# Performance work log

Hardware: AMD Instinct MI355X
Metric: run time of the kernel (lower is better)

The kernel has to match this reference:

```python
import jax, jax.numpy as jnp
import numpy as np

B, H_IMG, W_IMG, C_IMG, NP = 8, 384, 384, 3, 6
DELTA = 10
TOL = 1e-3
LAM = 0.05          # lambda_ (Charbonnier scale)
MAX_ITER = 12
RIDGE = 1e-6


def _cubic(s):
    # Keys bicubic convolution kernel, a = -0.5
    a = -0.5
    s = jnp.abs(s)
    s2 = s * s
    s3 = s2 * s
    w1 = (a + 2.0) * s3 - (a + 3.0) * s2 + 1.0
    w2 = a * s3 - 5.0 * a * s2 + 8.0 * a * s - 4.0 * a
    return jnp.where(s <= 1.0, w1, jnp.where(s < 2.0, w2, 0.0))


def _bicubic(I, xg, yg):
    # I: [b,H,W,C]; xg,yg: [b,H,W] sample coordinates
    Bn, Hh, Ww, C = I.shape
    x0 = jnp.floor(xg)
    y0 = jnp.floor(yg)
    tx = xg - x0
    ty = yg - y0
    xi = x0.astype(jnp.int32)
    yi = y0.astype(jnp.int32)
    bidx = jnp.arange(Bn)[:, None, None]
    out = jnp.zeros(I.shape, I.dtype)
    for j in range(4):           # fixed 4x4 tap stencil
        wy = _cubic(ty - (j - 1))
        yy = jnp.clip(yi + (j - 1), 0, Hh - 1)
        for k in range(4):
            wx = _cubic(tx - (k - 1))
            xx = jnp.clip(xi + (k - 1), 0, Ww - 1)
            out = out + (wy * wx)[..., None] * I[bidx, yy, xx, :]
    return out


def _params2matrix(p):
    # AFFINITY: x' = x + p0 + p2*x + p3*y ; y' = y + p1 + p4*x + p5*y
    zero = jnp.zeros_like(p[:, 0])
    one = jnp.ones_like(p[:, 0])
    r0 = jnp.stack([1.0 + p[:, 2], p[:, 3], p[:, 0]], -1)
    r1 = jnp.stack([p[:, 4], 1.0 + p[:, 5], p[:, 1]], -1)
    r2 = jnp.stack([zero, zero, one], -1)
    return jnp.stack([r0, r1, r2], 1)


def _matrix2params(M):
    M = M / M[:, 2:3, 2:3]
    return jnp.stack([M[:, 0, 2], M[:, 1, 2], M[:, 0, 0] - 1.0,
                      M[:, 0, 1], M[:, 1, 0], M[:, 1, 1] - 1.0], -1)


def _gradients(I):
    # central differences, zero-padded at the borders (as in compute_gradients)
    Ix = jnp.pad((I[:, :, 2:, :] - I[:, :, :-2, :]) * 0.5,
                 ((0, 0), (0, 0), (1, 1), (0, 0)))
    Iy = jnp.pad((I[:, 2:, :, :] - I[:, :-2, :, :]) * 0.5,
                 ((0, 0), (1, 1), (0, 0), (0, 0)))
    return Ix, Iy


def setup_inputs() -> dict:
    key = jax.random.key(0)
    k1, k2 = jax.random.split(key)
    I1 = jax.random.uniform(k1, (B, H_IMG, W_IMG, C_IMG), jnp.float32)
    I2 = jax.random.uniform(k2, (B, H_IMG, W_IMG, C_IMG), jnp.float32)
    p = jnp.zeros((B, NP), jnp.float32)
    return {"I1": I1, "I2": I2, "p": p}


def _forward(I1, I2, p):
    Bn, Hh, Ww, C = I1.shape
    x = jnp.arange(Ww, dtype=jnp.float32)
    y = jnp.arange(Hh, dtype=jnp.float32)
    X, Y = jnp.meshgrid(x, y)
    ones = jnp.ones_like(X)
    zeros = jnp.zeros_like(X)
    # AFFINITY Jacobian, split into Jx / Jy halves: [H,W,6]
    Jx = jnp.stack([ones, zeros, X, Y, zeros, zeros], -1)
    Jy = jnp.stack([zeros, ones, zeros, zeros, X, Y], -1)
    Ix, Iy = _gradients(I1)
    # steepest-descent images: [b,H,W,C,6]
    DIJ = Ix[..., None] * Jx[None, :, :, None, :] + Iy[..., None] * Jy[None, :, :, None, :]
    rows_ok = (jnp.arange(Hh) >= DELTA) & (jnp.arange(Hh) < Hh - DELTA)
    cols_ok = (jnp.arange(Ww) >= DELTA) & (jnp.arange(Ww) < Ww - DELTA)
    valid1 = (rows_ok[:, None] & cols_ok[None, :])[None, :, :, None]  # [1,H,W,1]
    coords = jnp.stack([X, Y, ones], 0)  # [3,H,W]
    eye = jnp.eye(NP, dtype=jnp.float32)

    def warp(pcur):
        M = _params2matrix(pcur)
        g = jnp.einsum('bij,jhw->bihw', M, coords)
        xg, yg = g[:, 0], g[:, 1]
        Iw = _bicubic(I2, xg, yg)
        gx = jnp.round(xg).astype(jnp.int32)
        gy = jnp.round(yg).astype(jnp.int32)
        wmask = ((gx >= DELTA) & (gx <= Ww - DELTA) &
                 (gy >= DELTA) & (gy <= Hh - DELTA))[..., None]
        return Iw, wmask

    def step(carry, _):
        pcur, done = carry
        Iw, wmask = carry_warp = warp(pcur)
        m = wmask & valid1
        DI = jnp.where(m, Iw - I1, 0.0)
        # Charbonnier influence weight psi(e) = 1/sqrt(1 + (e/lam)^2)
        w = jnp.where(m, jax.lax.rsqrt(1.0 + (DI / LAM) ** 2), 0.0)
        bvec = jnp.einsum('bhwcm,bhwc->bm', DIJ, w * DI)
        Hm = jnp.einsum('bhwcm,bhwcn->bmn', DIJ * w[..., None], DIJ)
        dp = jnp.linalg.solve(Hm + RIDGE * eye, bvec[..., None])[..., 0]
        # inverse-compositional update: W(p) <- W(p) o W(dp)^-1
        Mn = _params2matrix(pcur) @ jnp.linalg.inv(_params2matrix(dp))
        p_new = _matrix2params(Mn)
        conv = jnp.linalg.norm(dp, axis=-1) < TOL
        p_out = jnp.where(done[:, None], pcur, p_new)
        return (p_out, done | conv), None

    (pf, _), _ = jax.lax.scan(step, (p, jnp.zeros((Bn,), bool)), None, length=MAX_ITER)
    Iw, wmask = warp(pf)
    m = wmask & valid1
    DI = jnp.where(m, Iw - I1, 0.0)
    rho = 2.0 * LAM * LAM * (jnp.sqrt(1.0 + (DI / LAM) ** 2) - 1.0)
    mb = jnp.broadcast_to(m, DI.shape)
    cnt = jnp.sum(mb.astype(jnp.float32), axis=(1, 2, 3))
    err = jnp.sum(jnp.where(mb, rho, 0.0), axis=(1, 2, 3)) / jnp.maximum(cnt, 1.0)
    return pf, err, DI, Iw


def reference(I1, I2, p):
    return _forward(I1, I2, p)
```

## Files before the change

### kernel.cpp

```cpp
#include <hip/hip_runtime.h>
#include <math.h>

#define BB 8
#define HH 384
#define WW 384
#define NPAR 6
#define DEL 10
#define MAXIT 12
#define NACC 24
#define HWPIX (HH*WW)
#define NRT4 91
#define NWIN 6
#define NBX (NRT4*NWIN)
#define L1N 91
#define L1CNT (6*BB)
#define CNTS 92
#define NR2F 6
#define PITCHF 141
#define WSF 140
#define KB_ 8
#define SPS 32

typedef float vf4 __attribute__((ext_vector_type(4)));
typedef vf4 uvf4 __attribute__((aligned(4)));
typedef float f2v __attribute__((ext_vector_type(2), aligned(4)));
typedef float lf4 __attribute__((ext_vector_type(4)));

__device__ __forceinline__ vf4 ldv4(const float* p) { return *(const uvf4*)p; }

__device__ __forceinline__ lf4 ldpx3(const float* __restrict__ Ib, int pixoff) {
    const int fo = pixoff * 3;
    if (fo + 4 <= HWPIX * 3) {
        vf4 v = ldv4(Ib + fo);
        return (lf4){v.x, v.y, v.z, 0.f};
    }
    vf4 v = ldv4(Ib + fo - 1);
    return (lf4){v.y, v.z, v.w, 0.f};
}

__device__ __forceinline__ float cubicw(float s) {
    s = fabsf(s);
    float s2 = s * s, s3 = s2 * s;
    float w1 = 1.5f * s3 - 2.5f * s2 + 1.0f;
    float w2 = -0.5f * s3 + 2.5f * s2 - 4.0f * s + 2.0f;
    return (s <= 1.0f) ? w1 : ((s < 2.0f) ? w2 : 0.0f);
}

__device__ __forceinline__ void bicubic3_fast(const float* __restrict__ Ib, double xg, double yg, float Iw[3]) {
    double fx = floor(xg), fy = floor(yg);
    float tx = (float)(xg - fx), ty = (float)(yg - fy);
    int xi = (int)fx, yi = (int)fy;
    float wx[4], wyv[4];
#pragma unroll
    for (int k = 0; k < 4; k++) { wx[k] = cubicw(tx - (float)(k - 1)); wyv[k] = cubicw(ty - (float)(k - 1)); }
    Iw[0] = 0.f; Iw[1] = 0.f; Iw[2] = 0.f;
    const float* base = Ib + (yi - 1) * (WW * 3) + (xi - 1) * 3;
#pragma unroll
    for (int j = 0; j < 4; j++) {
        const float* r = base + j * (WW * 3);
        vf4 v0 = ldv4(r), v1 = ldv4(r + 4), v2 = ldv4(r + 8);
        float r0 = fmaf(wx[0], v0.x, 0.f); r0 = fmaf(wx[1], v0.w, r0); r0 = fmaf(wx[2], v1.z, r0); r0 = fmaf(wx[3], v2.y, r0);
        float r1 = fmaf(wx[0], v0.y, 0.f); r1 = fmaf(wx[1], v1.x, r1); r1 = fmaf(wx[2], v1.w, r1); r1 = fmaf(wx[3], v2.z, r1);
        float r2 = fmaf(wx[0], v0.z, 0.f); r2 = fmaf(wx[1], v1.y, r2); r2 = fmaf(wx[2], v2.x, r2); r2 = fmaf(wx[3], v2.w, r2);
        Iw[0] = fmaf(wyv[j], r0, Iw[0]);
        Iw[1] = fmaf(wyv[j], r1, Iw[1]);
        Iw[2] = fmaf(wyv[j], r2, Iw[2]);
    }
}

__device__ __forceinline__ void bicubic3_gen(const float* __restrict__ Ib, double xg, double yg, float Iw[3]) {
    double fx = floor(xg), fy = floor(yg);
    int xi = (int)fx, yi = (int)fy;
    float tx = (float)(xg - fx), ty = (float)(yg - fy);
    float wx[4], wyv[4];
    int xx[4], yy[4];
#pragma unroll
    for (int k = 0; k < 4; k++) {
        wx[k] = cubicw(tx - (float)(k - 1)); wyv[k] = cubicw(ty - (float)(k - 1));
        xx[k] = min(max(xi + k - 1, 0), WW - 1);
        yy[k] = min(max(yi + k - 1, 0), HH - 1);
    }
    Iw[0] = 0.f; Iw[1] = 0.f; Iw[2] = 0.f;
#pragma unroll
    for (int j = 0; j < 4; j++) {
        const float* row = Ib + yy[j] * (WW * 3);
        float r0 = 0.f, r1 = 0.f, r2 = 0.f;
#pragma unroll
        for (int k = 0; k < 4; k++) {
            const float* q = row + xx[k] * 3;
            r0 = fmaf(wx[k], q[0], r0); r1 = fmaf(wx[k], q[1], r1); r2 = fmaf(wx[k], q[2], r2);
        }
        Iw[0] = fmaf(wyv[j], r0, Iw[0]);
        Iw[1] = fmaf(wyv[j], r1, Iw[1]);
        Iw[2] = fmaf(wyv[j], r2, Iw[2]);
    }
}

template<int P>
__device__ __forceinline__ void bicubic3_lds(const lf4* __restrict__ T, int ssx, int ssy,
                                             float tx, float ty, float Iw[3]) {
    float wx[4], wyv[4];
#pragma unroll
    for (int k = 0; k < 4; k++) { wx[k] = cubicw(tx - (float)(k - 1)); wyv[k] = cubicw(ty - (float)(k - 1)); }
    Iw[0] = 0.f; Iw[1] = 0.f; Iw[2] = 0.f;
    const lf4* bp = T + (ssy - 1) * P + (ssx - 1);
#pragma unroll
    for (int j = 0; j < 4; j++) {
        lf4 t0 = bp[j * P + 0], t1 = bp[j * P + 1], t2 = bp[j * P + 2], t3 = bp[j * P + 3];
        float r0 = fmaf(wx[0], t0.x, 0.f); r0 = fmaf(wx[1], t1.x, r0); r0 = fmaf(wx[2], t2.x, r0); r0 = fmaf(wx[3], t3.x, r0);
        float r1 = fmaf(wx[0], t0.y, 0.f); r1 = fmaf(wx[1], t1.y, r1); r1 = fmaf(wx[2], t2.y, r1); r1 = fmaf(wx[3], t3.y, r1);
        float r2 = fmaf(wx[0], t0.z, 0.f); r2 = fmaf(wx[1], t1.z, r2); r2 = fmaf(wx[2], t2.z, r2); r2 = fmaf(wx[3], t3.z, r2);
        Iw[0] = fmaf(wyv[j], r0, Iw[0]);
        Iw[1] = fmaf(wyv[j], r1, Iw[1]);
        Iw[2] = fmaf(wyv[j], r2, Iw[2]);
    }
}

__device__ __forceinline__
void solve6_fast(const double* __restrict__ Sb, const double* __restrict__ pc,
                 double pn[6], int* convp) {
    const double b0 = Sb[0], b1 = Sb[3], b2 = Sb[1], b3 = Sb[2], b4 = Sb[4], b5 = Sb[5];
    const double h00 = Sb[6]  + 1e-6, h01 = Sb[12], h02 = Sb[7],  h03 = Sb[8],  h04 = Sb[13], h05 = Sb[14];
    const double h11 = Sb[18] + 1e-6, h12 = Sb[13], h13 = Sb[14], h14 = Sb[19], h15 = Sb[20];
    const double h22 = Sb[9]  + 1e-6, h23 = Sb[10], h24 = Sb[15], h25 = Sb[16];
    const double h33 = Sb[11] + 1e-6, h34 = Sb[16], h35 = Sb[17];
    const double h44 = Sb[21] + 1e-6, h45 = Sb[22];
    const double h55 = Sb[23] + 1e-6;

    const double l00 = sqrt(h00);
    const double i0 = 1.0 / l00;
    const double l10 = h01 * i0, l20 = h02 * i0, l30 = h03 * i0, l40 = h04 * i0, l50 = h05 * i0;
    const double l11 = sqrt(h11 - l10 * l10);
    const double i1 = 1.0 / l11;
    const double l21 = (h12 - l20 * l10) * i1;
    const double l31 = (h13 - l30 * l10) * i1;
    const double l41 = (h14 - l40 * l10) * i1;
    const double l51 = (h15 - l50 * l10) * i1;
    const double l22 = sqrt(h22 - l20 * l20 - l21 * l21);
    const double i2 = 1.0 / l22;
    const double l32 = (h23 - l30 * l20 - l31 * l21) * i2;
    const double l42 = (h24 - l40 * l20 - l41 * l21) * i2;
    const double l52 = (h25 - l50 * l20 - l51 * l21) * i2;
    const double l33 = sqrt(h33 - l30 * l30 - l31 * l31 - l32 * l32);
    const double i3 = 1.0 / l33;
    const double l43 = (h34 - l40 * l30 - l41 * l31 - l42 * l32) * i3;
    const double l53 = (h35 - l50 * l30 - l51 * l31 - l52 * l32) * i3;
    const double l44 = sqrt(h44 - l40 * l40 - l41 * l41 - l42 * l42 - l43 * l43);
    const double i4 = 1.0 / l44;
    const double l54 = (h45 - l50 * l40 - l51 * l41 - l52 * l42 - l53 * l43) * i4;
    const double l55 = sqrt(h55 - l50 * l50 - l51 * l51 - l52 * l52 - l53 * l53 - l54 * l54);
    const double i5 = 1.0 / l55;

    const double y0 = b0 * i0;
    const double y1 = (b1 - l10 * y0) * i1;
    const double y2 = (b2 - l20 * y0 - l21 * y1) * i2;
    const double y3 = (b3 - l30 * y0 - l31 * y1 - l32 * y2) * i3;
    const double y4 = (b4 - l40 * y0 - l41 * y1 - l42 * y2 - l43 * y3) * i4;
    const double y5 = (b5 - l50 * y0 - l51 * y1 - l52 * y2 - l53 * y3 - l54 * y4) * i5;

    const double d5 = y5 * i5;
    const double d4 = (y4 - l54 * d5) * i4;
    const double d3 = (y3 - l43 * d4 - l53 * d5) * i3;
    const double d2 = (y2 - l32 * d3 - l42 * d4 - l52 * d5) * i2;
    const double d1 = (y1 - l21 * d2 - l31 * d3 - l41 * d4 - l51 * d5) * i1;
    const double d0 = (y0 - l10 * d1 - l20 * d2 - l30 * d3 - l40 * d4 - l50 * d5) * i0;

    const double nrm = sqrt(d0*d0 + d1*d1 + d2*d2 + d3*d3 + d4*d4 + d5*d5);
    *convp = (nrm < 1e-3) ? 1 : 0;

    const double m00 = 1.0 + pc[2], m01 = pc[3], m02 = pc[0];
    const double m10 = pc[4], m11 = 1.0 + pc[5], m12 = pc[1];
    const double q00 = 1.0 + d2, q01 = d3, q02 = d0;
    const double q10 = d4, q11 = 1.0 + d5, q12 = d1;
    const double det = q00 * q11 - q01 * q10;
    const double j00 = q11 / det, j01 = -q01 / det;
    const double j10 = -q10 / det, j11 = q00 / det;
    const double jt0 = -(j00 * q02 + j01 * q12);
    const double jt1 = -(j10 * q02 + j11 * q12);
    const double n00 = m00 * j00 + m01 * j10;
    const double n01 = m00 * j01 + m01 * j11;
    const double n02 = m00 * jt0 + m01 * jt1 + m02;
    const double n10 = m10 * j00 + m11 * j10;
    const double n11 = m10 * j01 + m11 * j11;
    const double n12 = m10 * jt0 + m11 * jt1 + m12;
    pn[0] = n02;
    pn[1] = n12;
    pn[2] = n00 - 1.0;
    pn[3] = n01;
    pn[4] = n10;
    pn[5] = n11 - 1.0;
}

extern "C" __global__ __launch_bounds__(256)
void k_init(const float* __restrict__ p0, double* __restrict__ p_store,
            int* __restrict__ done0, double* __restrict__ S_part_all,
            double* __restrict__ Sf_part, unsigned int* __restrict__ cnt) {
    const int idx = blockIdx.x * 256 + threadIdx.x;
    const int n = MAXIT * KB_ * BB * SPS;
    for (int i = idx; i < n; i += gridDim.x * 256) S_part_all[i] = 0.0;
    for (int i = idx; i < MAXIT * CNTS; i += gridDim.x * 256) cnt[i] = 0u;
    if (blockIdx.x == 0) {
        const int tid = threadIdx.x;
        if (tid < KB_ * BB * 4) Sf_part[tid] = 0.0;
        if (tid < BB * NPAR) p_store[tid] = (double)p0[tid];
        if (tid < BB) done0[tid] = 0;
    }
}

extern "C" __global__ __launch_bounds__(256, 8)
void k_iter(const float* __restrict__ I1, const float* __restrict__ I2,
            const double* __restrict__ p_in, const int* __restrict__ done_in,
            double* __restrict__ S_out, double* __restrict__ p_out,
            int* __restrict__ done_out, unsigned int* __restrict__ c1,
            unsigned int* __restrict__ c2) {
    __shared__ __align__(16) double SMEMD[1664];
    __shared__ int lastflag;
    double* scr = SMEMD;
    const int tid = threadIdx.x;
    const int b = blockIdx.y;
    const int tix = blockIdx.x;
    const int dn = done_in[b];

    if (!dn) {
        const int rt = tix / NWIN, win = tix - rt * NWIN;
        const int y0 = 10 + rt * 4;
        const int x0 = 10 + win * 64;

        double pp[NPAR];
#pragma unroll
        for (int i = 0; i < NPAR; i++) pp[i] = p_in[b * NPAR + i];
        const double M00 = 1.0 + pp[2], M01 = pp[3], M02 = pp[0];
        const double M10 = pp[4], M11 = 1.0 + pp[5], M12 = pp[1];
        const float* I1b = I1 + (size_t)b * HWPIX * 3;
        const float* I2b = I2 + (size_t)b * HWPIX * 3;

        const int wid = tid >> 6, lane = tid & 63;
        const int y = y0 + wid;
        const double Y = (double)y;
        const double Bx = M01 * Y + M02;
        const double By = M11 * Y + M12;
        const int x = x0 + lane;
        const double X = (double)x;
        const double xg = fma(M00, X, Bx);
        const double yg = fma(M10, X, By);
        const double gx = rint(xg), gy = rint(yg);
        const bool ok = (x < WW - DEL) &&
                        (gx >= (double)DEL && gx <= (double)(WW - DEL) &&
                         gy >= (double)DEL && gy <= (double)(HH - DEL));

        float Iw[3];
        if (ok) {
            bicubic3_fast(I2b, xg, yg, Iw);
        } else {
            Iw[0] = 0.f; Iw[1] = 0.f; Iw[2] = 0.f;
        }

        const int xc = min(x, WW - DEL - 1);
        const int pixL = y * WW + xc;
        const float* c = I1b + pixL * 3;
        vf4 u0 = ldv4(c - 3);
        vf4 u1 = ldv4(c + 1);
        float cr2 = c[5];
        vf4 uu = ldv4(c - WW * 3);
        vf4 ud = ldv4(c + WW * 3);

        const float cl[3] = {u0.x, u0.y, u0.z};
        const float cv[3] = {u0.w, u1.x, u1.y};
        const float cr[3] = {u1.z, u1.w, cr2};
        const float cu[3] = {uu.x, uu.y, uu.z};
        const float cd[3] = {ud.x, ud.y, ud.z};

        const float msk = ok ? 1.0f : 0.0f;
        float Af = 0.f, Bf = 0.f, Cf = 0.f, T0f = 0.f, T1f = 0.f;
#pragma unroll
        for (int ch = 0; ch < 3; ch++) {
            const float Ix = (cr[ch] - cl[ch]) * 0.5f;
            const float Iy = (cd[ch] - cu[ch]) * 0.5f;
            const float d = Iw[ch] - cv[ch];
            const float u = d * 20.0f;
            const float w = msk / sqrtf(fmaf(u, u, 1.0f));
            const float wd = w * d;
            T0f = fmaf(Ix, wd, T0f);
            T1f = fmaf(Iy, wd, T1f);
            const float wIx = w * Ix;
            Af = fmaf(wIx, Ix, Af);
            Bf = fmaf(wIx, Iy, Bf);
            Cf = fmaf(w * Iy, Iy, Cf);
        }
        const double T0 = (double)T0f, T1 = (double)T1f;
        const double A = (double)Af, Bd = (double)Bf, Cd = (double)Cf;
        const double XX = X * X;
        double s[13];
        s[0] = T0;  s[1] = T0 * X;
        s[2] = T1;  s[3] = T1 * X;
        s[4] = A;   s[5] = A * X;   s[6] = A * XX;
        s[7] = Bd;  s[8] = Bd * X;  s[9] = Bd * XX;
        s[10] = Cd; s[11] = Cd * X; s[12] = Cd * XX;

#pragma unroll
        for (int i = 0; i < 13; i++) s[i] += __shfl_down(s[i], 32, 64);

        if (lane < 32) {
            double* o = scr + ((size_t)(wid * 32 + lane)) * 13;
#pragma unroll
            for (int i = 0; i < 13; i++) o[i] = s[i];
        }
        __syncthreads();

        if (tid < NACC) {
            const unsigned long long CLO = 0x9787456454232010ULL;
            const unsigned long long CHI = 0x00000000abcaba78ULL;
            const unsigned long long YPW = 0x0000910910910410ULL;
            const int cix = (int)(((tid < 16) ? (CLO >> (tid * 4)) : (CHI >> ((tid - 16) * 4))) & 0xF);
            const int pw  = (int)((YPW >> (tid * 2)) & 0x3);
            double acc = 0.0;
            for (int w = 0; w < 4; w++) {
                const double* basep = scr + ((size_t)(w * 32)) * 13 + cix;
                double part = 0.0;
                for (int l = 0; l < 32; l++) part += basep[(size_t)l * 13];
                const double Yw = (double)(y0 + w);
                const double f = (pw == 0) ? 1.0 : ((pw == 1) ? Yw : Yw * Yw);
                acc = fma(f, part, acc);
            }
            const int bkt = tix & (KB_ - 1);
            double oldv = unsafeAtomicAdd(&S_out[((size_t)(bkt * BB + b)) * SPS + tid], acc);
            asm volatile("" :: "v"(oldv));
        }
    }

    __syncthreads();
    if (tid == 0) {
        lastflag = 0;
        const unsigned o1 = __hip_atomic_fetch_add(&c1[tix % L1N], 1u,
                                __ATOMIC_RELAXED, __HIP_MEMORY_SCOPE_AGENT);
        if (o1 == (unsigned)(L1CNT - 1)) {
            const unsigned o2 = __hip_atomic_fetch_add(c2, 1u,
                                    __ATOMIC_RELAXED, __HIP_MEMORY_SCOPE_AGENT);
            if (o2 == (unsigned)(L1N - 1)) lastflag = 1;
        }
    }
    __syncthreads();
    if (lastflag) {
        double* FSUM = SMEMD;
        if (tid < BB * NACC) {
            const int bt = tid / NACC, a = tid - bt * NACC;
            double sv = 0.0;
#pragma unroll
            for (int k = 0; k < KB_; k++)
                sv += __hip_atomic_load(&S_out[((size_t)(k * BB + bt)) * SPS + a],
                                        __ATOMIC_RELAXED, __HIP_MEMORY_SCOPE_AGENT);
            FSUM[bt * NACC + a] = sv;
        }
        __syncthreads();
        if (tid < BB) {
            const int bt = tid;
            double pc[NPAR], pn[NPAR];
#pragma unroll
            for (int i = 0; i < NPAR; i++) pc[i] = p_in[bt * NPAR + i];
            if (done_in[bt]) {
#pragma unroll
                for (int i = 0; i < NPAR; i++) p_out[bt * NPAR + i] = pc[i];
                done_out[bt] = 1;
            } else {
                int conv;
                solve6_fast(&FSUM[bt * NACC], pc, pn, &conv);
#pragma unroll
                for (int i = 0; i < NPAR; i++) p_out[bt * NPAR + i] = pn[i];
                done_out[bt] = conv;
            }
        }
    }
}

extern "C" __global__ __launch_bounds__(256, 8)
void k_final_map(const float* __restrict__ I1, const float* __restrict__ I2,
                 const double* __restrict__ pf_in,
                 float* __restrict__ DI_out, float* __restrict__ Iw_out,
                 double* __restrict__ Sf_part) {
    __shared__ lf4 I2S[NR2F * PITCHF];
    __shared__ double wsum[4][2];
    const int tid = threadIdx.x;
    const int b = blockIdx.y;
    const int tix = blockIdx.x;
    const int rt = tix / 3, win = tix - rt * 3;
    const int y0 = rt * 2;
    const int x0 = win * 128;
    const int sx0 = x0 - 6;

    double pp[NPAR];
#pragma unroll
    for (int i = 0; i < NPAR; i++) pp[i] = pf_in[b * NPAR + i];
    const double M00 = 1.0 + pp[2], M01 = pp[3], M02 = pp[0];
    const double M10 = pp[4], M11 = 1.0 + pp[5], M12 = pp[1];
    const float* I1b = I1 + (size_t)b * HWPIX * 3;
    const float* I2b = I2 + (size_t)b * HWPIX * 3;
    float* DIb = DI_out + (size_t)b * HWPIX * 3;
    float* Iwb = Iw_out + (size_t)b * HWPIX * 3;

    const double ygc = M10 * (double)(x0 + 64) + M11 * ((double)y0 + 0.5) + M12;
    const int r0 = (int)fmin(fmax(floor(ygc) - 2.0, -100000.0), 100000.0);
    for (int i = tid; i < NR2F * WSF; i += 256) {
        const int r = i / WSF, c = i - r * WSF;
        const int gr = min(max(r0 + r, 0), HH - 1);
        const int gc = min(max(sx0 + c, 0), WW - 1);
        I2S[r * PITCHF + c] = ldpx3(I2b, gr * WW + gc);
    }
    __syncthreads();

    const int row = tid >> 7;
    const int x = x0 + (tid & 127);
    const int y = y0 + row;
    const int pix = y * WW + x;

    const double X = (double)x, Yd = (double)y;
    const double xg = fma(M00, X, fma(M01, Yd, M02));
    const double yg = fma(M10, X, fma(M11, Yd, M12));
    const double fx = floor(xg), fy = floor(yg);
    const int xi = (int)fx, yi = (int)fy;
    const float tx = (float)(xg - fx), ty = (float)(yg - fy);
    const int sxi = xi - sx0, syi = yi - r0;
    const bool inwin = (sxi >= 1) && (sxi <= WSF - 3) && (syi >= 1) && (syi <= NR2F - 3);

    float Iwp[3];
    if (inwin) bicubic3_lds<PITCHF>(I2S, sxi, syi, tx, ty, Iwp);
    else       bicubic3_gen(I2b, xg, yg, Iwp);

    const bool v1 = (x >= DEL) && (x < WW - DEL) && (y >= DEL) && (y < HH - DEL);
    const double gx = rint(xg), gy = rint(yg);
    const bool wm = (gx >= (double)DEL && gx <= (double)(WW - DEL) &&
                     gy >= (double)DEL && gy <= (double)(HH - DEL));
    const bool mp = v1 && wm;

    const float* cbase = I1b + (size_t)pix * 3;
    const float cv0 = cbase[0], cv1 = cbase[1], cv2 = cbase[2];

    {
        float* wp = Iwb + (size_t)pix * 3;
        *(f2v*)wp = (f2v){Iwp[0], Iwp[1]};
        wp[2] = Iwp[2];
    }
    double rho_s = 0.0, cnt_s = 0.0;
    {
        const float cvv[3] = {cv0, cv1, cv2};
        float dv[3];
#pragma unroll
        for (int ch = 0; ch < 3; ch++) {
            const float d1 = mp ? (Iwp[ch] - cvv[ch]) : 0.0f;
            dv[ch] = d1;
            if (mp) {
                const float u = d1 * 20.0f;
                rho_s += (double)(0.005f * (sqrtf(fmaf(u, u, 1.0f)) - 1.0f));
            }
        }
        if (mp) cnt_s += 3.0;
        float* dp_ = DIb + (size_t)pix * 3;
        *(f2v*)dp_ = (f2v){dv[0], dv[1]};
        dp_[2] = dv[2];
    }

#pragma unroll
    for (int off = 32; off >= 1; off >>= 1) {
        rho_s += __shfl_down(rho_s, off, 64);
        cnt_s += __shfl_down(cnt_s, off, 64);
    }
    const int wv = tid >> 6, lane = tid & 63;
    if (lane == 0) { wsum[wv][0] = rho_s; wsum[wv][1] = cnt_s; }
    __syncthreads();
    if (tid < 2) {
        double sv = wsum[0][tid] + wsum[1][tid] + wsum[2][tid] + wsum[3][tid];
        const int bkt = blockIdx.x & (KB_ - 1);
        unsafeAtomicAdd(&Sf_part[((size_t)(bkt * BB + b)) * 4 + tid], sv);
    }
}

extern "C" __global__ void k_finish(const double* __restrict__ p_fin,
                                    const double* __restrict__ Sf_part,
                                    float* __restrict__ out) {
    const int tid = threadIdx.x;
    if (tid < BB * NPAR) out[tid] = (float)p_fin[tid];
    if (tid >= 48 && tid < 48 + BB) {
        const int b = tid - 48;
        double rs = 0.0, cs = 0.0;
#pragma unroll
        for (int k = 0; k < KB_; k++) {
            rs += Sf_part[((size_t)(k * BB + b)) * 4 + 0];
            cs += Sf_part[((size_t)(k * BB + b)) * 4 + 1];
        }
        out[48 + b] = (float)(rs / fmax(cs, 1.0));
    }
}

extern "C" void kernel_launch(void* const* d_in, const int* in_sizes, int n_in,
                              void* d_out, int out_size, void* d_ws, size_t ws_size,
                              hipStream_t stream) {
    const float* I1 = (const float*)d_in[0];
    const float* I2 = (const float*)d_in[1];
    const float* p0 = (const float*)d_in[2];
    float* out = (float*)d_out;

    double* p_store = (double*)d_ws;
    int* done_flags = (int*)((char*)d_ws + 4992);
    double* S_part_all = (double*)((char*)d_ws + 5408);
    double* Sf_part = (double*)((char*)d_ws + 202016);
    unsigned int* cnt = (unsigned int*)((char*)d_ws + 204064);

    k_init<<<64, 256, 0, stream>>>(p0, p_store, done_flags, S_part_all, Sf_part, cnt);

    const size_t SIT = (size_t)KB_ * BB * SPS;
    dim3 gridI(NBX, BB), blkI(256);
    for (int it = 0; it < MAXIT; it++) {
        k_iter<<<gridI, blkI, 0, stream>>>(I1, I2,
                                           p_store + (size_t)it * BB * NPAR,
                                           done_flags + it * BB,
                                           S_part_all + (size_t)it * SIT,
                                           p_store + (size_t)(it + 1) * BB * NPAR,
                                           done_flags + (it + 1) * BB,
                                           cnt + it * CNTS,
                                           cnt + it * CNTS + L1N);
    }
    float* DI_out = out + 56;
    float* Iw_out = out + 56 + (size_t)BB * HWPIX * 3;
    dim3 gridF(192 * 3, BB), blkF(256);
    k_final_map<<<gridF, blkF, 0, stream>>>(I1, I2,
                                            p_store + (size_t)MAXIT * BB * NPAR,
                                            DI_out, Iw_out, Sf_part);
    k_finish<<<1, 64, 0, stream>>>(p_store + (size_t)MAXIT * BB * NPAR, Sf_part, out);
}
```

Measured before the change: 427.6 us.

## Halve iter grid with two-strip loop and fold finish into final map

```diff
diff --git a/kernel.cpp b/kernel.cpp
--- a/kernel.cpp
+++ b/kernel.cpp
@@ -10,11 +10,14 @@
 #define NACC 24
 #define HWPIX (HH*WW)
 #define NRT4 91
-#define NWIN 6
-#define NBX (NRT4*NWIN)
+#define NWP 3
+#define NBX (NRT4*NWP)
 #define L1N 91
-#define L1CNT (6*BB)
+#define L1CNT (NWP*BB)
 #define CNTS 92
+#define CF1N 96
+#define CF1CNT (6*BB)
+#define CNT_TOTAL (MAXIT*CNTS + CF1N + 1)
 #define NR2F 6
 #define PITCHF 141
 #define WSF 140
@@ -198,7 +201,7 @@
     const int idx = blockIdx.x * 256 + threadIdx.x;
     const int n = MAXIT * KB_ * BB * SPS;
     for (int i = idx; i < n; i += gridDim.x * 256) S_part_all[i] = 0.0;
-    for (int i = idx; i < MAXIT * CNTS; i += gridDim.x * 256) cnt[i] = 0u;
+    for (int i = idx; i < CNT_TOTAL; i += gridDim.x * 256) cnt[i] = 0u;
     if (blockIdx.x == 0) {
         const int tid = threadIdx.x;
         if (tid < KB_ * BB * 4) Sf_part[tid] = 0.0;
@@ -222,9 +225,9 @@
     const int dn = done_in[b];
 
     if (!dn) {
-        const int rt = tix / NWIN, win = tix - rt * NWIN;
+        const int rt = tix / NWP, wp = tix - rt * NWP;
         const int y0 = 10 + rt * 4;
-        const int x0 = 10 + win * 64;
+        const int x0b = 10 + wp * 128;
 
         double pp[NPAR];
 #pragma unroll
@@ -239,71 +242,80 @@
         const double Y = (double)y;
         const double Bx = M01 * Y + M02;
         const double By = M11 * Y + M12;
-        const int x = x0 + lane;
-        const double X = (double)x;
-        const double xg = fma(M00, X, Bx);
-        const double yg = fma(M10, X, By);
-        const double gx = rint(xg), gy = rint(yg);
-        const bool ok = (x < WW - DEL) &&
-                        (gx >= (double)DEL && gx <= (double)(WW - DEL) &&
-                         gy >= (double)DEL && gy <= (double)(HH - DEL));
-
-        float Iw[3];
-        if (ok) {
-            bicubic3_fast(I2b, xg, yg, Iw);
-        } else {
-            Iw[0] = 0.f; Iw[1] = 0.f; Iw[2] = 0.f;
-        }
-
-        const int xc = min(x, WW - DEL - 1);
-        const int pixL = y * WW + xc;
-        const float* c = I1b + pixL * 3;
-        vf4 u0 = ldv4(c - 3);
-        vf4 u1 = ldv4(c + 1);
-        float cr2 = c[5];
-        vf4 uu = ldv4(c - WW * 3);
-        vf4 ud = ldv4(c + WW * 3);
-
-        const float cl[3] = {u0.x, u0.y, u0.z};
-        const float cv[3] = {u0.w, u1.x, u1.y};
-        const float cr[3] = {u1.z, u1.w, cr2};
-        const float cu[3] = {uu.x, uu.y, uu.z};
-        const float cd[3] = {ud.x, ud.y, ud.z};
-
-        const float msk = ok ? 1.0f : 0.0f;
-        float Af = 0.f, Bf = 0.f, Cf = 0.f, T0f = 0.f, T1f = 0.f;
-#pragma unroll
-        for (int ch = 0; ch < 3; ch++) {
-            const float Ix = (cr[ch] - cl[ch]) * 0.5f;
-            const float Iy = (cd[ch] - cu[ch]) * 0.5f;
-            const float d = Iw[ch] - cv[ch];
-            const float u = d * 20.0f;
-            const float w = msk / sqrtf(fmaf(u, u, 1.0f));
-            const float wd = w * d;
-            T0f = fmaf(Ix, wd, T0f);
-            T1f = fmaf(Iy, wd, T1f);
-            const float wIx = w * Ix;
-            Af = fmaf(wIx, Ix, Af);
-            Bf = fmaf(wIx, Iy, Bf);
-            Cf = fmaf(w * Iy, Iy, Cf);
-        }
-        const double T0 = (double)T0f, T1 = (double)T1f;
-        const double A = (double)Af, Bd = (double)Bf, Cd = (double)Cf;
-        const double XX = X * X;
-        double s[13];
-        s[0] = T0;  s[1] = T0 * X;
-        s[2] = T1;  s[3] = T1 * X;
-        s[4] = A;   s[5] = A * X;   s[6] = A * XX;
-        s[7] = Bd;  s[8] = Bd * X;  s[9] = Bd * XX;
-        s[10] = Cd; s[11] = Cd * X; s[12] = Cd * XX;
-
-#pragma unroll
-        for (int i = 0; i < 13; i++) s[i] += __shfl_down(s[i], 32, 64);
-
-        if (lane < 32) {
-            double* o = scr + ((size_t)(wid * 32 + lane)) * 13;
-#pragma unroll
-            for (int i = 0; i < 13; i++) o[i] = s[i];
+        double* o = scr + ((size_t)(wid * 32 + lane & 31) * 0);
+        o = scr + ((size_t)(wid * 32 + (lane & 31))) * 13;
+
+#pragma unroll 1
+        for (int h = 0; h < 2; h++) {
+            const int x = x0b + h * 64 + lane;
+            const double X = (double)x;
+            const double xg = fma(M00, X, Bx);
+            const double yg = fma(M10, X, By);
+            const double gx = rint(xg), gy = rint(yg);
+            const bool ok = (x < WW - DEL) &&
+                            (gx >= (double)DEL && gx <= (double)(WW - DEL) &&
+                             gy >= (double)DEL && gy <= (double)(HH - DEL));
+
+            float Iw[3];
+            if (ok) {
+                bicubic3_fast(I2b, xg, yg, Iw);
+            } else {
+                Iw[0] = 0.f; Iw[1] = 0.f; Iw[2] = 0.f;
+            }
+
+            const int xc = min(x, WW - DEL - 1);
+            const int pixL = y * WW + xc;
+            const float* c = I1b + pixL * 3;
+            vf4 u0 = ldv4(c - 3);
+            vf4 u1 = ldv4(c + 1);
+            float cr2 = c[5];
+            vf4 uu = ldv4(c - WW * 3);
+            vf4 ud = ldv4(c + WW * 3);
+
+            const float cl[3] = {u0.x, u0.y, u0.z};
+            const float cv[3] = {u0.w, u1.x, u1.y};
+            const float cr[3] = {u1.z, u1.w, cr2};
+            const float cu[3] = {uu.x, uu.y, uu.z};
+            const float cd[3] = {ud.x, ud.y, ud.z};
+
+            const float msk = ok ? 1.0f : 0.0f;
+            float Af = 0.f, Bf = 0.f, Cf = 0.f, T0f = 0.f, T1f = 0.f;
+#pragma unroll
+            for (int ch = 0; ch < 3; ch++) {
+                const float Ix = (cr[ch] - cl[ch]) * 0.5f;
+                const float Iy = (cd[ch] - cu[ch]) * 0.5f;
+                const float d = Iw[ch] - cv[ch];
+                const float u = d * 20.0f;
+                const float w = msk / sqrtf(fmaf(u, u, 1.0f));
+                const float wd = w * d;
+                T0f = fmaf(Ix, wd, T0f);
+                T1f = fmaf(Iy, wd, T1f);
+                const float wIx = w * Ix;
+                Af = fmaf(wIx, Ix, Af);
+                Bf = fmaf(wIx, Iy, Bf);
+                Cf = fmaf(w * Iy, Iy, Cf);
+            }
+            const double T0 = (double)T0f, T1 = (double)T1f;
+            const double A = (double)Af, Bd = (double)Bf, Cd = (double)Cf;
+            const double XX = X * X;
+            double s[13];
+            s[0] = T0;  s[1] = T0 * X;
+            s[2] = T1;  s[3] = T1 * X;
+            s[4] = A;   s[5] = A * X;   s[6] = A * XX;
+            s[7] = Bd;  s[8] = Bd * X;  s[9] = Bd * XX;
+            s[10] = Cd; s[11] = Cd * X; s[12] = Cd * XX;
+
+#pragma unroll
+            for (int i = 0; i < 13; i++) s[i] += __shfl_down(s[i], 32, 64);
+            if (lane < 32) {
+                if (h == 0) {
+#pragma unroll
+                    for (int i = 0; i < 13; i++) o[i] = s[i];
+                } else {
+#pragma unroll
+                    for (int i = 0; i < 13; i++) o[i] += s[i];
+                }
+            }
         }
         __syncthreads();
 
@@ -376,9 +388,11 @@
 void k_final_map(const float* __restrict__ I1, const float* __restrict__ I2,
                  const double* __restrict__ pf_in,
                  float* __restrict__ DI_out, float* __restrict__ Iw_out,
-                 double* __restrict__ Sf_part) {
+                 double* __restrict__ Sf_part, float* __restrict__ out_head,
+                 unsigned int* __restrict__ c1f, unsigned int* __restrict__ c2f) {
     __shared__ lf4 I2S[NR2F * PITCHF];
     __shared__ double wsum[4][2];
+    __shared__ int lastflag;
     const int tid = threadIdx.x;
     const int b = blockIdx.y;
     const int tix = blockIdx.x;
@@ -469,24 +483,36 @@
     if (tid < 2) {
         double sv = wsum[0][tid] + wsum[1][tid] + wsum[2][tid] + wsum[3][tid];
         const int bkt = blockIdx.x & (KB_ - 1);
-        unsafeAtomicAdd(&Sf_part[((size_t)(bkt * BB + b)) * 4 + tid], sv);
-    }
-}
-
-extern "C" __global__ void k_finish(const double* __restrict__ p_fin,
-                                    const double* __restrict__ Sf_part,
-                                    float* __restrict__ out) {
-    const int tid = threadIdx.x;
-    if (tid < BB * NPAR) out[tid] = (float)p_fin[tid];
-    if (tid >= 48 && tid < 48 + BB) {
-        const int b = tid - 48;
-        double rs = 0.0, cs = 0.0;
-#pragma unroll
-        for (int k = 0; k < KB_; k++) {
-            rs += Sf_part[((size_t)(k * BB + b)) * 4 + 0];
-            cs += Sf_part[((size_t)(k * BB + b)) * 4 + 1];
-        }
-        out[48 + b] = (float)(rs / fmax(cs, 1.0));
+        double ov = unsafeAtomicAdd(&Sf_part[((size_t)(bkt * BB + b)) * 4 + tid], sv);
+        asm volatile("" :: "v"(ov));
+    }
+
+    __syncthreads();
+    if (tid == 0) {
+        lastflag = 0;
+        const unsigned o1 = __hip_atomic_fetch_add(&c1f[tix % CF1N], 1u,
+                                __ATOMIC_RELAXED, __HIP_MEMORY_SCOPE_AGENT);
+        if (o1 == (unsigned)(CF1CNT - 1)) {
+            const unsigned o2 = __hip_atomic_fetch_add(c2f, 1u,
+                                    __ATOMIC_RELAXED, __HIP_MEMORY_SCOPE_AGENT);
+            if (o2 == (unsigned)(CF1N - 1)) lastflag = 1;
+        }
+    }
+    __syncthreads();
+    if (lastflag && tid < 64) {
+        if (tid < BB * NPAR) out_head[tid] = (float)pf_in[tid];
+        if (tid >= 48 && tid < 48 + BB) {
+            const int bt = tid - 48;
+            double rs = 0.0, cs = 0.0;
+#pragma unroll
+            for (int k = 0; k < KB_; k++) {
+                rs += __hip_atomic_load(&Sf_part[((size_t)(k * BB + bt)) * 4 + 0],
+                                        __ATOMIC_RELAXED, __HIP_MEMORY_SCOPE_AGENT);
+                cs += __hip_atomic_load(&Sf_part[((size_t)(k * BB + bt)) * 4 + 1],
+                                        __ATOMIC_RELAXED, __HIP_MEMORY_SCOPE_AGENT);
+            }
+            out_head[48 + bt] = (float)(rs / fmax(cs, 1.0));
+        }
     }
 }
 
@@ -520,9 +546,10 @@
     }
     float* DI_out = out + 56;
     float* Iw_out = out + 56 + (size_t)BB * HWPIX * 3;
+    unsigned int* cf = cnt + MAXIT * CNTS;
     dim3 gridF(192 * 3, BB), blkF(256);
     k_final_map<<<gridF, blkF, 0, stream>>>(I1, I2,
                                             p_store + (size_t)MAXIT * BB * NPAR,
-                                            DI_out, Iw_out, Sf_part);
-    k_finish<<<1, 64, 0, stream>>>(p_store + (size_t)MAXIT * BB * NPAR, Sf_part, out);
-}
+                                            DI_out, Iw_out, Sf_part, out,
+                                            cf, cf + CF1N);
+}
```

After: 488.4 us. +14.2%, slower.
